# Kernel optimization log

Hardware: AMD Instinct MI355X
Metric: run time of the kernel (lower is better)

The kernel has to match this reference:

```python
import jax, jax.numpy as jnp
import numpy as np

UNITS = 2048
RHO = 0.99          # spectral_radius
LEAKY = 1.0         # leaky integration coefficient
INPUT_SCALING = 1.0
BIAS_SCALING = 1.0
B, T, D_IN = 32, 512, 128


def setup_inputs() -> dict:
    key = jax.random.key(0)
    k1, k2, k3 = jax.random.split(key, 3)
    inputs = jax.random.normal(k1, (B, T, D_IN), dtype=jnp.float32)
    h0 = jnp.zeros((B, UNITS), dtype=jnp.float32)
    # original uses deterministic +/-1 signs from pi digits; same structure: sign matrix * scaling
    kernel = jnp.where(jax.random.uniform(k2, (D_IN, UNITS)) >= 0.5, 1.0, -1.0).astype(jnp.float32) * INPUT_SCALING
    bias = jnp.where(jax.random.uniform(k3, (UNITS,)) >= 0.5, 1.0, -1.0).astype(jnp.float32) * BIAS_SCALING
    return {"inputs": inputs, "h0": h0, "kernel": kernel, "bias": bias}


def reference(inputs, h0, kernel, bias):
    # Precompute input projection for all timesteps: [B, T, U]
    u = jnp.einsum("btd,du->btu", inputs, kernel)

    def step(h, u_t):
        # prev @ recurrent_kernel == spectral_radius * cyclic shift of prev
        state_part = RHO * jnp.roll(h, 1, axis=-1)
        h_new = h * (1.0 - LEAKY) + jnp.tanh(u_t + bias + state_part) * LEAKY
        return h_new, h_new

    _, ys = jax.lax.scan(step, h0, jnp.swapaxes(u, 0, 1))  # scan over time
    return jnp.swapaxes(ys, 0, 1)  # [B, T, U]
```

## Files before the change

kernel.cpp:

```cpp
#include <hip/hip_runtime.h>
#include <hip/hip_bf16.h>

#define U_ 2048
#define T_ 512
#define K_ 128
#define B_ 32
#define RHO_ 0.99f
#define CPB 128
#define NTILES 9
#define NSLOTS 10
#define NIT (T_ / 16)

typedef __attribute__((ext_vector_type(8))) short short8;
typedef __attribute__((ext_vector_type(4))) float f32x4;

__device__ __forceinline__ unsigned short bf16_rne(float x) {
  unsigned int u = __float_as_uint(x);
  u += 0x7FFFu + ((u >> 16) & 1u);
  return (unsigned short)(u >> 16);
}

#define GLOAD_LDS16(gsrc, ldst)                                        \
  __builtin_amdgcn_global_load_lds(                                    \
      (const __attribute__((address_space(1))) void*)(gsrc),           \
      (__attribute__((address_space(3))) void*)(ldst), 16, 0, 0)

__global__ __launch_bounds__(256) void convert_a_kernel(
    const float* __restrict__ A, unsigned short* __restrict__ Ab) {
  const int gi = blockIdx.x * 256 + threadIdx.x;
  const int m = gi >> 5;
  const int kq = (gi & 31) << 2;
  const float4 v = *(const float4*)&A[(size_t)m * K_ + kq];
  ushort4 hi, lo;
  hi.x = bf16_rne(v.x); hi.y = bf16_rne(v.y); hi.z = bf16_rne(v.z); hi.w = bf16_rne(v.w);
  lo.x = bf16_rne(v.x - __uint_as_float((unsigned)hi.x << 16));
  lo.y = bf16_rne(v.y - __uint_as_float((unsigned)hi.y << 16));
  lo.z = bf16_rne(v.z - __uint_as_float((unsigned)hi.z << 16));
  lo.w = bf16_rne(v.w - __uint_as_float((unsigned)hi.w << 16));
  *(ushort4*)&Ab[(size_t)m * 256 + kq] = hi;
  *(ushort4*)&Ab[(size_t)m * 256 + 128 + kq] = lo;
}

__global__ __launch_bounds__(256) void convert_w_kernel(
    const float* __restrict__ W, unsigned short* __restrict__ Wbt) {
  const int gi = blockIdx.x * 256 + threadIdx.x;
  const int kq = gi >> 11;
  const int n = gi & 2047;
  const int k = kq << 2;
  ushort4 w;
  w.x = bf16_rne(W[(size_t)(k + 0) * U_ + n]);
  w.y = bf16_rne(W[(size_t)(k + 1) * U_ + n]);
  w.z = bf16_rne(W[(size_t)(k + 2) * U_ + n]);
  w.w = bf16_rne(W[(size_t)(k + 3) * U_ + n]);
  *(ushort4*)&Wbt[(size_t)n * 256 + k] = w;
  *(ushort4*)&Wbt[(size_t)n * 256 + 128 + k] = w;
}

__global__ __launch_bounds__(256, 2) void fused_gemm_scan6_kernel(
    const unsigned short* __restrict__ Ab, const unsigned short* __restrict__ Wbt,
    const float* __restrict__ bias, const float* __restrict__ h0,
    float* __restrict__ out) {
  __shared__ unsigned short Wl[NSLOTS * 2048];
  __shared__ unsigned short Al[2][4096];
  __shared__ float u_lds[2][16 * 146];
  const int tid = threadIdx.x;
  const int id = blockIdx.x + (blockIdx.y << 4);
  const int xcd = id & 7;
  const int wk = id >> 3;
  const int b = (xcd << 2) + (wk >> 4);
  const int bx = wk & 15;
  const int c0 = bx << 7;
  const int cbase = bx << 3;
  const int wave = tid >> 6;
  const int lane = tid & 63;
  const int r = lane & 15;
  const int q = lane >> 4;
  const bool producer = (wave >= 2);
  const int ptid = tid & 127;

  const unsigned short* const aBase = Ab + (((size_t)b * T_) << 8);

  if (producer) {
    #pragma unroll
    for (int k = 0; k < 4; ++k) {
      const int p = ptid + (k << 7);
      const int row = p >> 5, pg = p & 31;
      GLOAD_LDS16(aBase + ((size_t)row << 8) + ((pg ^ (row & 7)) << 3),
                  &Al[0][p << 3]);
    }
    #pragma unroll
    for (int j = 0; j < NTILES; ++j) {
      const int g = (cbase + j) & 127;
      #pragma unroll
      for (int k = 0; k < 2; ++k) {
        const int p = ptid + (k << 7);
        const int row = p >> 4, pg = p & 15;
        GLOAD_LDS16(Wbt + ((size_t)((g << 4) + row) << 8) + ((pg ^ (row & 7)) << 3),
                    &Wl[(j << 11) + (p << 3)]);
      }
    }
  }
  float h_prev = 0.0f;
  float hreg[16];
  if (!producer)
    h_prev = h0[((size_t)b << 11) + ((c0 + tid + U_ - 1) & (U_ - 1))];

  __syncthreads();

  const int isw2 = (wave == 2) ? 1 : 0;

  for (int it = 0; it < NIT; ++it) {
    const int cur = it & 1;
    const int t0 = it << 4;

    if (producer) {
      if (it + 1 < NIT) {
        #pragma unroll
        for (int k = 0; k < 4; ++k) {
          const int p = ptid + (k << 7);
          const int row = p >> 5, pg = p & 31;
          GLOAD_LDS16(aBase + ((size_t)(t0 + 16 + row) << 8) + ((pg ^ (row & 7)) << 3),
                      &Al[cur ^ 1][p << 3]);
        }
        const int g = (cbase + it + NTILES) & 127;
        const int snew = (it + NTILES) % NSLOTS;
        #pragma unroll
        for (int k = 0; k < 2; ++k) {
          const int p = ptid + (k << 7);
          const int row = p >> 4, pg = p & 15;
          GLOAD_LDS16(Wbt + ((size_t)((g << 4) + row) << 8) + ((pg ^ (row & 7)) << 3),
                      &Wl[(snew << 11) + (p << 3)]);
        }
      }
      float bvv[5];
      #pragma unroll
      for (int u = 0; u < 5; ++u) {
        if (u < 4 || isw2) {
          const int j = (u < 4) ? ((isw2 ? 0 : 4) + u) : 8;
          bvv[u] = bias[(((cbase + it + j) & 127) << 4) + r];
        }
      }
      short8 af[8];
      #pragma unroll
      for (int ks = 0; ks < 8; ++ks)
        af[ks] = *(const short8*)&Al[cur][(r << 8) + ((((ks << 2) + q) ^ (r & 7)) << 3)];
      #pragma unroll
      for (int u = 0; u < 5; ++u) {
        if (u < 4 || isw2) {
          const int j = (u < 4) ? ((isw2 ? 0 : 4) + u) : 8;
          const int slot = (it + j) % NSLOTS;
          short8 bfk[4];
          #pragma unroll
          for (int ks = 0; ks < 4; ++ks)
            bfk[ks] = *(const short8*)&Wl[(slot << 11) + (r << 7) +
                                          ((((ks << 2) + q) ^ (r & 7)) << 3)];
          f32x4 acc = (f32x4){0.f, 0.f, 0.f, 0.f};
          #pragma unroll
          for (int ks = 0; ks < 8; ++ks)
            acc = __builtin_amdgcn_mfma_f32_16x16x32_bf16(af[ks], bfk[ks & 3], acc, 0, 0, 0);
          #pragma unroll
          for (int reg = 0; reg < 4; ++reg)
            u_lds[cur][((q << 2) + reg) * 146 + (j << 4) + r] = acc[reg] + bvv[u];
        }
      }
      asm volatile("s_waitcnt vmcnt(0) lgkmcnt(0)\n\ts_barrier" ::: "memory");
      __builtin_amdgcn_sched_barrier(0);
    } else {
      if (it > 0) {
        const int t0p = t0 - 16;
        float* const orow = out + (((size_t)(b * T_ + t0p)) << 11);
        #pragma unroll
        for (int tt = 0; tt < 16; ++tt)
          __builtin_nontemporal_store(
              hreg[tt], &orow[((size_t)tt << 11) + ((c0 + tid + t0p + tt) & (U_ - 1))]);
      }
      asm volatile("s_waitcnt lgkmcnt(0)\n\ts_barrier" ::: "memory");
      __builtin_amdgcn_sched_barrier(0);
      float uv[16];
      #pragma unroll
      for (int tt = 0; tt < 16; ++tt)
        uv[tt] = u_lds[cur][tt * 146 + tid + tt];
      float x = fmaf(RHO_, h_prev, uv[0]);
      #pragma unroll
      for (int tt = 0; tt < 16; ++tt) {
        float e = __builtin_amdgcn_exp2f(2.8853900817779268f * x);
        float rc = __builtin_amdgcn_rcpf(e + 1.0f);
        hreg[tt] = fmaf(-2.0f, rc, 1.0f);
        if (tt < 15) x = fmaf(-2.0f * RHO_, rc, uv[tt + 1] + RHO_);
      }
      h_prev = hreg[15];
    }
  }

  if (!producer) {
    const int t0p = T_ - 16;
    float* const orow = out + (((size_t)(b * T_ + t0p)) << 11);
    #pragma unroll
    for (int tt = 0; tt < 16; ++tt)
      __builtin_nontemporal_store(
          hreg[tt], &orow[((size_t)tt << 11) + ((c0 + tid + t0p + tt) & (U_ - 1))]);
  }
}

__device__ __forceinline__ float fast_tanh(float x) {
  float e = __builtin_amdgcn_exp2f(2.8853900817779268f * x);
  return 1.0f - 2.0f * __builtin_amdgcn_rcpf(e + 1.0f);
}

__global__ __launch_bounds__(256) void ring_scan_kernel(
    float* __restrict__ buf, const float* __restrict__ h0) {
  const int b = blockIdx.y;
  const int c = (blockIdx.x << 8) + threadIdx.x;
  float* const base = buf + (size_t)b * (T_ * U_);
  float h = h0[((size_t)b << 11) + ((c + U_ - 1) & (U_ - 1))];
  float wA[8], wB[8];
  #pragma unroll
  for (int j = 0; j < 8; ++j)
    wA[j] = base[((size_t)j << 11) + ((c + j) & (U_ - 1))];
  for (int t0 = 0; t0 < T_; t0 += 16) {
    #pragma unroll
    for (int j = 0; j < 8; ++j) {
      const int t = t0 + 8 + j;
      wB[j] = base[((size_t)t << 11) + ((c + t) & (U_ - 1))];
    }
    #pragma unroll
    for (int j = 0; j < 8; ++j) {
      const int t = t0 + j;
      h = fast_tanh(fmaf(RHO_, h, wA[j]));
      base[((size_t)t << 11) + ((c + t) & (U_ - 1))] = h;
    }
    if (t0 + 16 < T_) {
      #pragma unroll
      for (int j = 0; j < 8; ++j) {
        const int t = t0 + 16 + j;
        wA[j] = base[((size_t)t << 11) + ((c + t) & (U_ - 1))];
      }
    }
    #pragma unroll
    for (int j = 0; j < 8; ++j) {
      const int t = t0 + 8 + j;
      h = fast_tanh(fmaf(RHO_, h, wB[j]));
      base[((size_t)t << 11) + ((c + t) & (U_ - 1))] = h;
    }
  }
}

__global__ __launch_bounds__(256, 4) void gemm_bias_kernel(
    const float* __restrict__ A, const float* __restrict__ W,
    const float* __restrict__ bias, float* __restrict__ out) {
  __shared__ float Asf[64][68];
  __shared__ float Bsf[64][64];
  const int tid = threadIdx.x;
  const int m0 = blockIdx.y << 6;
  const int n0 = blockIdx.x << 6;
  const int tx = tid & 15;
  const int ty = tid >> 4;
  float acc[4][4] = {};
  #pragma unroll
  for (int kb = 0; kb < 2; ++kb) {
    if (kb) __syncthreads();
    {
      const int c4 = tid & 15;
      const int r0 = tid >> 4;
      #pragma unroll
      for (int rr = 0; rr < 4; ++rr) {
        const int r = r0 + (rr << 4);
        const float4 v = *(const float4*)(A + (size_t)(m0 + r) * K_ + (kb << 6) + (c4 << 2));
        Asf[(c4 << 2) + 0][r] = v.x;
        Asf[(c4 << 2) + 1][r] = v.y;
        Asf[(c4 << 2) + 2][r] = v.z;
        Asf[(c4 << 2) + 3][r] = v.w;
      }
    }
    {
      const int c4 = tid & 15;
      const int r0 = tid >> 4;
      #pragma unroll
      for (int rr = 0; rr < 4; ++rr) {
        const int k = r0 + (rr << 4);
        *(float4*)&Bsf[k][c4 << 2] =
            *(const float4*)(W + (size_t)((kb << 6) + k) * U_ + n0 + (c4 << 2));
      }
    }
    __syncthreads();
    #pragma unroll 16
    for (int k = 0; k < 64; ++k) {
      const float4 a = *(const float4*)&Asf[k][ty << 2];
      const float4 b = *(const float4*)&Bsf[k][tx << 2];
      acc[0][0] = fmaf(a.x, b.x, acc[0][0]); acc[0][1] = fmaf(a.x, b.y, acc[0][1]);
      acc[0][2] = fmaf(a.x, b.z, acc[0][2]); acc[0][3] = fmaf(a.x, b.w, acc[0][3]);
      acc[1][0] = fmaf(a.y, b.x, acc[1][0]); acc[1][1] = fmaf(a.y, b.y, acc[1][1]);
      acc[1][2] = fmaf(a.y, b.z, acc[1][2]); acc[1][3] = fmaf(a.y, b.w, acc[1][3]);
      acc[2][0] = fmaf(a.z, b.x, acc[2][0]); acc[2][1] = fmaf(a.z, b.y, acc[2][1]);
      acc[2][2] = fmaf(a.z, b.z, acc[2][2]); acc[2][3] = fmaf(a.z, b.w, acc[2][3]);
      acc[3][0] = fmaf(a.w, b.x, acc[3][0]); acc[3][1] = fmaf(a.w, b.y, acc[3][1]);
      acc[3][2] = fmaf(a.w, b.z, acc[3][2]); acc[3][3] = fmaf(a.w, b.w, acc[3][3]);
    }
  }
  const float4 bv = *(const float4*)(bias + n0 + (tx << 2));
  #pragma unroll
  for (int i = 0; i < 4; ++i) {
    float4 o;
    o.x = acc[i][0] + bv.x; o.y = acc[i][1] + bv.y;
    o.z = acc[i][2] + bv.z; o.w = acc[i][3] + bv.w;
    *(float4*)(out + (size_t)(m0 + (ty << 2) + i) * U_ + n0 + (tx << 2)) = o;
  }
}

extern "C" void kernel_launch(void* const* d_in, const int* in_sizes, int n_in,
                              void* d_out, int out_size, void* d_ws, size_t ws_size,
                              hipStream_t stream) {
  const float* A    = (const float*)d_in[0];
  const float* h0   = (const float*)d_in[1];
  const float* W    = (const float*)d_in[2];
  const float* bias = (const float*)d_in[3];
  float* out = (float*)d_out;

  const size_t AB_BYTES = (size_t)B_ * T_ * 256 * 2;
  const size_t WB_BYTES = (size_t)U_ * 256 * 2;
  const size_t NEEDED = AB_BYTES + WB_BYTES;

  if (ws_size >= NEEDED) {
    unsigned short* Ab  = (unsigned short*)d_ws;
    unsigned short* Wbt = (unsigned short*)((char*)d_ws + AB_BYTES);

    convert_a_kernel<<<2048, 256, 0, stream>>>(A, Ab);
    convert_w_kernel<<<256, 256, 0, stream>>>(W, Wbt);
    dim3 fg(U_ / CPB, B_);
    fused_gemm_scan6_kernel<<<fg, 256, 0, stream>>>(Ab, Wbt, bias, h0, out);
  } else {
    dim3 gemm_grid(U_ / 64, (B_ * T_) / 64);
    gemm_bias_kernel<<<gemm_grid, 256, 0, stream>>>(A, W, bias, out);
    dim3 scan_grid(U_ / 256, B_);
    ring_scan_kernel<<<scan_grid, 256, 0, stream>>>(out, h0);
  }
}
```

Before: 182.3 us.

## Fuse input hi/lo bf16 split into the fused GEMM-scan producer waves

Removes the separate convert_a kernel and its 8 MB bf16 workspace round-trip. Producer waves now load fp32 input rows through registers, split them into hi/lo bf16 in-kernel, and write them to the swizzled LDS A buffer after the MFMA work, so the load overlaps compute. This trades one kernel launch and extra global traffic for more producer VALU work and register pressure, plus synchronous register loads in place of direct global-to-LDS copies.

```diff
diff --git a/kernel.cpp b/kernel.cpp
--- a/kernel.cpp
+++ b/kernel.cpp
@@ -20,26 +20,21 @@
   return (unsigned short)(u >> 16);
 }
 
+__device__ __forceinline__ void cvt_hilo(const float4 va, const float4 vb,
+                                         short8* hi, short8* lo) {
+  const float f[8] = {va.x, va.y, va.z, va.w, vb.x, vb.y, vb.z, vb.w};
+  #pragma unroll
+  for (int i = 0; i < 8; ++i) {
+    const unsigned short h = bf16_rne(f[i]);
+    (*hi)[i] = (short)h;
+    (*lo)[i] = (short)bf16_rne(f[i] - __uint_as_float((unsigned)h << 16));
+  }
+}
+
 #define GLOAD_LDS16(gsrc, ldst)                                        \
   __builtin_amdgcn_global_load_lds(                                    \
       (const __attribute__((address_space(1))) void*)(gsrc),           \
       (__attribute__((address_space(3))) void*)(ldst), 16, 0, 0)
-
-__global__ __launch_bounds__(256) void convert_a_kernel(
-    const float* __restrict__ A, unsigned short* __restrict__ Ab) {
-  const int gi = blockIdx.x * 256 + threadIdx.x;
-  const int m = gi >> 5;
-  const int kq = (gi & 31) << 2;
-  const float4 v = *(const float4*)&A[(size_t)m * K_ + kq];
-  ushort4 hi, lo;
-  hi.x = bf16_rne(v.x); hi.y = bf16_rne(v.y); hi.z = bf16_rne(v.z); hi.w = bf16_rne(v.w);
-  lo.x = bf16_rne(v.x - __uint_as_float((unsigned)hi.x << 16));
-  lo.y = bf16_rne(v.y - __uint_as_float((unsigned)hi.y << 16));
-  lo.z = bf16_rne(v.z - __uint_as_float((unsigned)hi.z << 16));
-  lo.w = bf16_rne(v.w - __uint_as_float((unsigned)hi.w << 16));
-  *(ushort4*)&Ab[(size_t)m * 256 + kq] = hi;
-  *(ushort4*)&Ab[(size_t)m * 256 + 128 + kq] = lo;
-}
 
 __global__ __launch_bounds__(256) void convert_w_kernel(
     const float* __restrict__ W, unsigned short* __restrict__ Wbt) {
@@ -56,8 +51,8 @@
   *(ushort4*)&Wbt[(size_t)n * 256 + 128 + k] = w;
 }
 
-__global__ __launch_bounds__(256, 2) void fused_gemm_scan6_kernel(
-    const unsigned short* __restrict__ Ab, const unsigned short* __restrict__ Wbt,
+__global__ __launch_bounds__(256, 2) void fused_gemm_scan8_kernel(
+    const float* __restrict__ A, const unsigned short* __restrict__ Wbt,
     const float* __restrict__ bias, const float* __restrict__ h0,
     float* __restrict__ out) {
   __shared__ unsigned short Wl[NSLOTS * 2048];
@@ -77,17 +72,12 @@
   const int q = lane >> 4;
   const bool producer = (wave >= 2);
   const int ptid = tid & 127;
-
-  const unsigned short* const aBase = Ab + (((size_t)b * T_) << 8);
+  const int arow0 = ptid >> 4, afg0 = ptid & 15, apg0 = afg0 ^ (arow0 & 7);
+  const int arow1 = 8 + arow0, apg1 = afg0 ^ (arow1 & 7);
+
+  const float* const aBaseF = A + (size_t)b * T_ * K_;
 
   if (producer) {
-    #pragma unroll
-    for (int k = 0; k < 4; ++k) {
-      const int p = ptid + (k << 7);
-      const int row = p >> 5, pg = p & 31;
-      GLOAD_LDS16(aBase + ((size_t)row << 8) + ((pg ^ (row & 7)) << 3),
-                  &Al[0][p << 3]);
-    }
     #pragma unroll
     for (int j = 0; j < NTILES; ++j) {
       const int g = (cbase + j) & 127;
@@ -99,6 +89,17 @@
                     &Wl[(j << 11) + (p << 3)]);
       }
     }
+    {
+      const float* s0 = aBaseF + (size_t)arow0 * K_ + (afg0 << 3);
+      const float* s1 = aBaseF + (size_t)arow1 * K_ + (afg0 << 3);
+      short8 hi, lo;
+      cvt_hilo(*(const float4*)s0, *(const float4*)(s0 + 4), &hi, &lo);
+      *(short8*)&Al[0][(arow0 << 8) + (apg0 << 3)] = hi;
+      *(short8*)&Al[0][(arow0 << 8) + ((16 + apg0) << 3)] = lo;
+      cvt_hilo(*(const float4*)s1, *(const float4*)(s1 + 4), &hi, &lo);
+      *(short8*)&Al[0][(arow1 << 8) + (apg1 << 3)] = hi;
+      *(short8*)&Al[0][(arow1 << 8) + ((16 + apg1) << 3)] = lo;
+    }
   }
   float h_prev = 0.0f;
   float hreg[16];
@@ -114,14 +115,12 @@
     const int t0 = it << 4;
 
     if (producer) {
+      float4 a00, a01, a10, a11;
       if (it + 1 < NIT) {
-        #pragma unroll
-        for (int k = 0; k < 4; ++k) {
-          const int p = ptid + (k << 7);
-          const int row = p >> 5, pg = p & 31;
-          GLOAD_LDS16(aBase + ((size_t)(t0 + 16 + row) << 8) + ((pg ^ (row & 7)) << 3),
-                      &Al[cur ^ 1][p << 3]);
-        }
+        const float* s0 = aBaseF + (size_t)(t0 + 16 + arow0) * K_ + (afg0 << 3);
+        const float* s1 = aBaseF + (size_t)(t0 + 16 + arow1) * K_ + (afg0 << 3);
+        a00 = *(const float4*)s0; a01 = *(const float4*)(s0 + 4);
+        a10 = *(const float4*)s1; a11 = *(const float4*)(s1 + 4);
         const int g = (cbase + it + NTILES) & 127;
         const int snew = (it + NTILES) % NSLOTS;
         #pragma unroll
@@ -163,6 +162,15 @@
             u_lds[cur][((q << 2) + reg) * 146 + (j << 4) + r] = acc[reg] + bvv[u];
         }
       }
+      if (it + 1 < NIT) {
+        short8 hi, lo;
+        cvt_hilo(a00, a01, &hi, &lo);
+        *(short8*)&Al[cur ^ 1][(arow0 << 8) + (apg0 << 3)] = hi;
+        *(short8*)&Al[cur ^ 1][(arow0 << 8) + ((16 + apg0) << 3)] = lo;
+        cvt_hilo(a10, a11, &hi, &lo);
+        *(short8*)&Al[cur ^ 1][(arow1 << 8) + (apg1 << 3)] = hi;
+        *(short8*)&Al[cur ^ 1][(arow1 << 8) + ((16 + apg1) << 3)] = lo;
+      }
       asm volatile("s_waitcnt vmcnt(0) lgkmcnt(0)\n\ts_barrier" ::: "memory");
       __builtin_amdgcn_sched_barrier(0);
     } else {
@@ -316,18 +324,14 @@
   const float* bias = (const float*)d_in[3];
   float* out = (float*)d_out;
 
-  const size_t AB_BYTES = (size_t)B_ * T_ * 256 * 2;
   const size_t WB_BYTES = (size_t)U_ * 256 * 2;
-  const size_t NEEDED = AB_BYTES + WB_BYTES;
-
-  if (ws_size >= NEEDED) {
-    unsigned short* Ab  = (unsigned short*)d_ws;
-    unsigned short* Wbt = (unsigned short*)((char*)d_ws + AB_BYTES);
-
-    convert_a_kernel<<<2048, 256, 0, stream>>>(A, Ab);
+
+  if (ws_size >= WB_BYTES) {
+    unsigned short* Wbt = (unsigned short*)d_ws;
+
     convert_w_kernel<<<256, 256, 0, stream>>>(W, Wbt);
     dim3 fg(U_ / CPB, B_);
-    fused_gemm_scan6_kernel<<<fg, 256, 0, stream>>>(Ab, Wbt, bias, h0, out);
+    fused_gemm_scan8_kernel<<<fg, 256, 0, stream>>>(A, Wbt, bias, h0, out);
   } else {
     dim3 gemm_grid(U_ / 64, (B_ * T_) / 64);
     gemm_bias_kernel<<<gemm_grid, 256, 0, stream>>>(A, W, bias, out);
```

After: 201.5 us. +10.5%, slower.
